# Kernel optimization log

Hardware: AMD Instinct MI355X
Metric: run time of the kernel (lower is better)

## Reference

```python
import jax, jax.numpy as jnp
import numpy as np

EMBED_DIM = 1024
NUM_HEADS = 16
HEAD_DIM = EMBED_DIM // NUM_HEADS


def setup_inputs() -> dict:
    key = jax.random.key(0)
    ks = jax.random.split(key, 9)
    s = 1.0 / np.sqrt(EMBED_DIM)
    inp = {"x": jax.random.normal(ks[0], (2, 2048, EMBED_DIM), dtype=jnp.float32)}
    for i, name in enumerate(["q", "k", "v", "out"]):
        inp[f"W_{name}"] = jax.random.uniform(ks[1 + 2 * i], (EMBED_DIM, EMBED_DIM), jnp.float32, -s, s)
        inp[f"b_{name}"] = jax.random.uniform(ks[2 + 2 * i], (EMBED_DIM,), jnp.float32, -s, s)
    return inp


def _heads(x):
    # [B, S, D] -> [B, H, S, Dh]
    b, s, _ = x.shape
    return x.reshape(b, s, NUM_HEADS, HEAD_DIM).transpose(0, 2, 1, 3)


def reference(x, W_q, b_q, W_k, b_k, W_v, b_v, W_out, b_out):
    q = _heads(x @ W_q.T + b_q)
    k = _heads(x @ W_k.T + b_k)
    v = _heads(x @ W_v.T + b_v)
    scale = HEAD_DIM ** 0.5
    logits = jnp.einsum("bhqd,bhkd->bhqk", q, k) / scale  # [B,H,S,S]
    s = x.shape[1]
    causal = jnp.tril(jnp.ones((s, s), dtype=bool))
    logits = jnp.where(causal, logits, -jnp.inf)
    a = jax.nn.softmax(logits, axis=-1)
    o = jnp.einsum("bhqk,bhkd->bhqd", a, v)
    o = o.transpose(0, 2, 1, 3).reshape(x.shape[0], s, EMBED_DIM)
    return o @ W_out.T + b_out
```

## Files before the change

### kernel.cpp

```cpp
#include <hip/hip_runtime.h>
#include <hip/hip_bf16.h>

typedef __bf16 bf16_t;
typedef __bf16 bf16x8 __attribute__((ext_vector_type(8)));
typedef __bf16 bf16x4 __attribute__((ext_vector_type(4)));
typedef float  f32x4  __attribute__((ext_vector_type(4)));

#define MFMA16(a, b, c) __builtin_amdgcn_mfma_f32_16x16x32_bf16((a), (b), (c), 0, 0, 0)

constexpr int E  = 1024;
constexpr int S  = 2048;
constexpr int H  = 16;
constexpr int M  = 4096;

__device__ __forceinline__ void glds16(const bf16_t* src, bf16_t* dst) {
  __builtin_amdgcn_global_load_lds(
      (const __attribute__((address_space(1))) void*)src,
      (__attribute__((address_space(3))) void*)dst, 16, 0, 0);
}

template <int ROWS, int NT>
__device__ __forceinline__ void stage_tile(const bf16_t* g, int gld,
                                           bf16_t* lds, int tid) {
  const int w = tid >> 6, l = tid & 63;
#pragma unroll
  for (int i = 0; i < ROWS * 8 / NT; ++i) {
    const int c = i * NT + w * 64 + l;
    const int row = c >> 3;
    const int gch = (c & 7) ^ (row & 7);
    glds16(g + (size_t)row * gld + gch * 8, lds + (size_t)(i * NT + w * 64) * 8);
  }
}

__device__ __forceinline__ bf16x8 read_frag(const bf16_t* lds, int row, int kc) {
  return *(const bf16x8*)(lds + (size_t)((row << 3) + (kc ^ (row & 7))) * 8);
}

__global__ void cvt_all_kernel(const float* __restrict__ x,
                               const float* __restrict__ w0, const float* __restrict__ w1,
                               const float* __restrict__ w2, const float* __restrict__ w3,
                               bf16_t* __restrict__ xb,
                               bf16_t* __restrict__ o0, bf16_t* __restrict__ o1,
                               bf16_t* __restrict__ o2, bf16_t* __restrict__ o3) {
  const int bid = blockIdx.x;
  const float* s;
  bf16_t* d;
  int idx;
  if (bid < 4096) {
    s = x; d = xb; idx = bid * 256 + threadIdx.x;
  } else {
    const int seg = (bid - 4096) >> 10;
    s = seg == 0 ? w0 : seg == 1 ? w1 : seg == 2 ? w2 : w3;
    d = seg == 0 ? o0 : seg == 1 ? o1 : seg == 2 ? o2 : o3;
    idx = ((bid - 4096) & 1023) * 256 + threadIdx.x;
  }
  float4 v = ((const float4*)s)[idx];
  bf16x4 o;
  o[0] = (bf16_t)v.x; o[1] = (bf16_t)v.y; o[2] = (bf16_t)v.z; o[3] = (bf16_t)v.w;
  ((bf16x4*)d)[idx] = o;
}

__device__ __forceinline__ void gemm_core(const bf16_t* __restrict__ A,
                                          const bf16_t* __restrict__ W, int Kd,
                                          bf16_t* As, bf16_t* Bs, int tid,
                                          f32x4 acc[4][4]) {
  const int w = tid >> 6, l = tid & 63;
  const int lq = l & 15, qd = l >> 4;
  const int wr = (w >> 1) * 64, wc = (w & 1) * 64;
#pragma unroll
  for (int i = 0; i < 4; ++i)
#pragma unroll
    for (int j = 0; j < 4; ++j) acc[i][j] = (f32x4){0.f, 0.f, 0.f, 0.f};

  const int KT = Kd / 64;
  for (int kt = 0; kt < KT; ++kt) {
    __syncthreads();
    stage_tile<128, 256>(A + kt * 64, Kd, As, tid);
    stage_tile<128, 256>(W + kt * 64, Kd, Bs, tid);
    __syncthreads();
#pragma unroll
    for (int ks = 0; ks < 2; ++ks) {
      bf16x8 af[4], bw[4];
#pragma unroll
      for (int mi = 0; mi < 4; ++mi)
        af[mi] = read_frag(As, wr + mi * 16 + lq, ks * 4 + qd);
#pragma unroll
      for (int ni = 0; ni < 4; ++ni)
        bw[ni] = read_frag(Bs, wc + ni * 16 + lq, ks * 4 + qd);
#pragma unroll
      for (int mi = 0; mi < 4; ++mi)
#pragma unroll
        for (int ni = 0; ni < 4; ++ni)
          acc[mi][ni] = MFMA16(af[mi], bw[ni], acc[mi][ni]);
    }
  }
}

__global__ __launch_bounds__(256) void qkv_gemm_kernel(
    const bf16_t* __restrict__ xb,
    const bf16_t* __restrict__ wq, const bf16_t* __restrict__ wk,
    const bf16_t* __restrict__ wv,
    const float* __restrict__ bq, const float* __restrict__ bk,
    const float* __restrict__ bv,
    bf16_t* __restrict__ Qb, bf16_t* __restrict__ Kb, bf16_t* __restrict__ Vb) {
  __shared__ __align__(16) bf16_t As[128 * 64];
  __shared__ __align__(16) bf16_t Bs[128 * 64];
  const int tid = threadIdx.x;
  const int which = blockIdx.x >> 3;
  const int n0 = (blockIdx.x & 7) * 128;
  const int m0 = blockIdx.y * 128;
  const bf16_t* Wp = which == 0 ? wq : which == 1 ? wk : wv;
  const float* bp  = which == 0 ? bq : which == 1 ? bk : bv;
  bf16_t* Out      = which == 0 ? Qb : which == 1 ? Kb : Vb;
  const float sc = (which == 0) ? (1.4426950408889634f * 0.125f) : 1.0f;

  f32x4 acc[4][4];
  gemm_core(xb + (size_t)m0 * E, Wp + (size_t)n0 * E, E, As, Bs, tid, acc);

  const int w = tid >> 6, l = tid & 63, lq = l & 15, qd = l >> 4;
  const int wr = (w >> 1) * 64, wc = (w & 1) * 64;
#pragma unroll
  for (int ni = 0; ni < 4; ++ni) {
    const int col = n0 + wc + ni * 16 + lq;
    const float bvv = bp[col];
#pragma unroll
    for (int mi = 0; mi < 4; ++mi)
#pragma unroll
      for (int r = 0; r < 4; ++r) {
        const int row = m0 + wr + mi * 16 + qd * 4 + r;
        Out[(size_t)row * E + col] = (bf16_t)((acc[mi][ni][r] + bvv) * sc);
      }
  }
}

__global__ __launch_bounds__(256) void vtrans_kernel(const bf16_t* __restrict__ Vb,
                                                     bf16_t* __restrict__ VT) {
  constexpr int LDT = 72;
  __shared__ __align__(16) bf16_t T[64 * LDT];
  const int tid = threadIdx.x;
  const int st = blockIdx.x, bh = blockIdx.y;
  const int b = bh >> 4, h = bh & 15;
  const int s0 = st * 64;
  const size_t rowbase = (size_t)b * S;
#pragma unroll
  for (int i = 0; i < 2; ++i) {
    const int c = i * 256 + tid;
    const int sl = c >> 3, dp = c & 7;
    const int a = sl >> 4, bb = (sl >> 2) & 3, cc = sl & 3;
    const int p = (a >> 1) * 32 + bb * 8 + (a & 1) * 4 + cc;
    bf16x8 v = *(const bf16x8*)(Vb + (rowbase + s0 + sl) * E + h * 64 + dp * 8);
    *(bf16x8*)&T[p * LDT + dp * 8] = v;
  }
  __syncthreads();
#pragma unroll
  for (int i = 0; i < 2; ++i) {
    const int c = i * 256 + tid;
    const int d = c >> 3, pp = (c & 7) * 8;
    bf16x8 o;
#pragma unroll
    for (int j = 0; j < 8; ++j) o[j] = T[(pp + j) * LDT + d];
    *(bf16x8*)&VT[((size_t)bh * 64 + d) * S + s0 + pp] = o;
  }
}

__global__ __launch_bounds__(256) void oproj_gemm_kernel(
    const bf16_t* __restrict__ Ob, const bf16_t* __restrict__ wo,
    const float* __restrict__ bo, float* __restrict__ out) {
  __shared__ __align__(16) bf16_t As[64 * 64];
  __shared__ __align__(16) bf16_t Bs[128 * 64];
  const int tid = threadIdx.x;
  const int n0 = blockIdx.x * 128;
  const int m0 = blockIdx.y * 64;
  const int w = tid >> 6, l = tid & 63, lq = l & 15, qd = l >> 4;
  const int wr = (w >> 1) * 32, wc = (w & 1) * 64;

  f32x4 acc[2][4];
#pragma unroll
  for (int i = 0; i < 2; ++i)
#pragma unroll
    for (int j = 0; j < 4; ++j) acc[i][j] = (f32x4){0.f, 0.f, 0.f, 0.f};

  for (int kt = 0; kt < 16; ++kt) {
    __syncthreads();
    stage_tile<64, 256>(Ob + (size_t)m0 * E + kt * 64, E, As, tid);
    stage_tile<128, 256>(wo + (size_t)n0 * E + kt * 64, E, Bs, tid);
    __syncthreads();
#pragma unroll
    for (int ks = 0; ks < 2; ++ks) {
      bf16x8 af[2], bw[4];
#pragma unroll
      for (int mi = 0; mi < 2; ++mi)
        af[mi] = read_frag(As, wr + mi * 16 + lq, ks * 4 + qd);
#pragma unroll
      for (int ni = 0; ni < 4; ++ni)
        bw[ni] = read_frag(Bs, wc + ni * 16 + lq, ks * 4 + qd);
#pragma unroll
      for (int mi = 0; mi < 2; ++mi)
#pragma unroll
        for (int ni = 0; ni < 4; ++ni)
          acc[mi][ni] = MFMA16(af[mi], bw[ni], acc[mi][ni]);
    }
  }
#pragma unroll
  for (int ni = 0; ni < 4; ++ni) {
    const int col = n0 + wc + ni * 16 + lq;
    const float bvv = bo[col];
#pragma unroll
    for (int mi = 0; mi < 2; ++mi)
#pragma unroll
      for (int r = 0; r < 4; ++r) {
        const int row = m0 + wr + mi * 16 + qd * 4 + r;
        out[(size_t)row * E + col] = acc[mi][ni][r] + bvv;
      }
  }
}

__global__ __launch_bounds__(128, 2) void attn_kernel(
    const bf16_t* __restrict__ Q, const bf16_t* __restrict__ K,
    const bf16_t* __restrict__ VT, bf16_t* __restrict__ O) {
  __shared__ __align__(16) bf16_t Ks[2][64 * 64];
  __shared__ __align__(16) bf16_t Vt[2][64 * 64];

  const int tid = threadIdx.x;
  const int w = tid >> 6, l = tid & 63;
  const int lq = l & 15, qd = l >> 4;
  const int bid = blockIdx.x;
  const int g = bid & 7, t = bid >> 3;
  const int bh = g * 4 + (t & 3);
  const int qt = 31 - (t >> 2);
  const int b = bh >> 4, h = bh & 15;
  const int qr = qt * 64 + w * 32;
  const size_t rowbase = (size_t)b * S;
  const size_t vtbase = (size_t)bh * 64 * S;
  const bf16_t* Kg = K + rowbase * E + h * 64;
  const bf16_t* Vg = VT + vtbase;

  stage_tile<64, 128>(Kg, E, Ks[0], tid);
  stage_tile<64, 128>(Vg, S, Vt[0], tid);

  bf16x8 aq[2][2];
#pragma unroll
  for (int mi = 0; mi < 2; ++mi)
#pragma unroll
    for (int ks = 0; ks < 2; ++ks)
      aq[mi][ks] = *(const bf16x8*)(Q + (rowbase + qr + mi * 16 + lq) * E +
                                    h * 64 + ks * 32 + qd * 8);

  f32x4 oacc[2][4];
#pragma unroll
  for (int mi = 0; mi < 2; ++mi)
#pragma unroll
    for (int nt = 0; nt < 4; ++nt) oacc[mi][nt] = (f32x4){0.f, 0.f, 0.f, 0.f};
  float rs[2] = {0.f, 0.f};

  for (int kt = 0; kt <= qt; ++kt) {
    __syncthreads();
    if (kt < qt) {
      const int kn = (kt + 1) * 64;
      stage_tile<64, 128>(Kg + (size_t)kn * E, E, Ks[(kt + 1) & 1], tid);
      stage_tile<64, 128>(Vg + kn, S, Vt[(kt + 1) & 1], tid);
    }
    const bf16_t* Kc = Ks[kt & 1];
    const bf16_t* Vc = Vt[kt & 1];
    const int k0 = kt * 64;
    const bool needmask = (k0 + 63 > qr);

    f32x4 sacc[2][4];
#pragma unroll
    for (int mi = 0; mi < 2; ++mi)
#pragma unroll
      for (int nt = 0; nt < 4; ++nt) sacc[mi][nt] = (f32x4){0.f, 0.f, 0.f, 0.f};
#pragma unroll
    for (int ks = 0; ks < 2; ++ks) {
      bf16x8 bk[4];
#pragma unroll
      for (int nt = 0; nt < 4; ++nt)
        bk[nt] = read_frag(Kc, nt * 16 + lq, ks * 4 + qd);
#pragma unroll
      for (int mi = 0; mi < 2; ++mi)
#pragma unroll
        for (int nt = 0; nt < 4; ++nt)
          sacc[mi][nt] = MFMA16(bk[nt], aq[mi][ks], sacc[mi][nt]);
    }
    bf16x8 ap[2][2];
#pragma unroll
    for (int mi = 0; mi < 2; ++mi) {
#pragma unroll
      for (int nt = 0; nt < 4; ++nt)
#pragma unroll
        for (int r = 0; r < 4; ++r) {
          float pv = exp2f(sacc[mi][nt][r]);
          if (needmask) {
            const int kg = k0 + nt * 16 + qd * 4 + r;
            const int qg = qr + mi * 16 + lq;
            pv = (kg > qg) ? 0.f : pv;
          }
          rs[mi] += pv;
          ap[mi][nt >> 1][((nt & 1) << 2) | r] = (bf16_t)pv;
        }
    }
#pragma unroll
    for (int ks = 0; ks < 2; ++ks) {
      bf16x8 bv[4];
#pragma unroll
      for (int nt = 0; nt < 4; ++nt)
        bv[nt] = read_frag(Vc, nt * 16 + lq, ks * 4 + qd);
#pragma unroll
      for (int mi = 0; mi < 2; ++mi)
#pragma unroll
        for (int nt = 0; nt < 4; ++nt)
          oacc[mi][nt] = MFMA16(ap[mi][ks], bv[nt], oacc[mi][nt]);
    }
  }

#pragma unroll
  for (int mi = 0; mi < 2; ++mi) {
    float tt = rs[mi];
    tt += __shfl_xor(tt, 16);
    tt += __shfl_xor(tt, 32);
    rs[mi] = tt;
  }
#pragma unroll
  for (int mi = 0; mi < 2; ++mi) {
    float rinv[4];
#pragma unroll
    for (int r = 0; r < 4; ++r)
      rinv[r] = 1.0f / __shfl(rs[mi], qd * 4 + r);
#pragma unroll
    for (int nt = 0; nt < 4; ++nt)
#pragma unroll
      for (int r = 0; r < 4; ++r) {
        const int qg = qr + mi * 16 + qd * 4 + r;
        O[(rowbase + qg) * E + h * 64 + nt * 16 + lq] =
            (bf16_t)(oacc[mi][nt][r] * rinv[r]);
      }
  }
}

extern "C" void kernel_launch(void* const* d_in, const int* in_sizes, int n_in,
                              void* d_out, int out_size, void* d_ws, size_t ws_size,
                              hipStream_t stream) {
  const float* x  = (const float*)d_in[0];
  const float* Wq = (const float*)d_in[1];
  const float* bq = (const float*)d_in[2];
  const float* Wk = (const float*)d_in[3];
  const float* bk = (const float*)d_in[4];
  const float* Wv = (const float*)d_in[5];
  const float* bv = (const float*)d_in[6];
  const float* Wo = (const float*)d_in[7];
  const float* bo = (const float*)d_in[8];
  float* out = (float*)d_out;

  unsigned char* ws = (unsigned char*)d_ws;
  constexpr size_t MB = 1ull << 20;
  bf16_t* xb  = (bf16_t*)(ws + 0 * MB);
  bf16_t* wqb = (bf16_t*)(ws + 8 * MB);
  bf16_t* wkb = (bf16_t*)(ws + 10 * MB);
  bf16_t* wvb = (bf16_t*)(ws + 12 * MB);
  bf16_t* wob = (bf16_t*)(ws + 14 * MB);
  bf16_t* Qb  = (bf16_t*)(ws + 16 * MB);
  bf16_t* Kb  = (bf16_t*)(ws + 24 * MB);
  bf16_t* Vb  = (bf16_t*)(ws + 32 * MB);
  bf16_t* VT  = (bf16_t*)(ws + 40 * MB);
  bf16_t* Ob  = xb;

  cvt_all_kernel<<<4096 + 4 * 1024, 256, 0, stream>>>(
      x, Wq, Wk, Wv, Wo, xb, wqb, wkb, wvb, wob);

  qkv_gemm_kernel<<<dim3(24, 32), 256, 0, stream>>>(
      xb, wqb, wkb, wvb, bq, bk, bv, Qb, Kb, Vb);

  vtrans_kernel<<<dim3(32, 32), 256, 0, stream>>>(Vb, VT);

  attn_kernel<<<1024, 128, 0, stream>>>(Qb, Kb, VT, Ob);

  oproj_gemm_kernel<<<dim3(8, 64), 256, 0, stream>>>(Ob, wob, bo, out);
}
```

Baseline: 208.8 us.

## Pair causal query tiles per block and use four waves of 16 rows

```diff
diff --git a/kernel.cpp b/kernel.cpp
--- a/kernel.cpp
+++ b/kernel.cpp
@@ -215,7 +215,7 @@
   }
 }
 
-__global__ __launch_bounds__(128, 2) void attn_kernel(
+__global__ __launch_bounds__(256, 2) void attn_kernel(
     const bf16_t* __restrict__ Q, const bf16_t* __restrict__ K,
     const bf16_t* __restrict__ VT, bf16_t* __restrict__ O) {
   __shared__ __align__(16) bf16_t Ks[2][64 * 64];
@@ -227,112 +227,100 @@
   const int bid = blockIdx.x;
   const int g = bid & 7, t = bid >> 3;
   const int bh = g * 4 + (t & 3);
-  const int qt = 31 - (t >> 2);
+  const int p = t >> 2;
   const int b = bh >> 4, h = bh & 15;
-  const int qr = qt * 64 + w * 32;
   const size_t rowbase = (size_t)b * S;
-  const size_t vtbase = (size_t)bh * 64 * S;
   const bf16_t* Kg = K + rowbase * E + h * 64;
-  const bf16_t* Vg = VT + vtbase;
-
-  stage_tile<64, 128>(Kg, E, Ks[0], tid);
-  stage_tile<64, 128>(Vg, S, Vt[0], tid);
-
-  bf16x8 aq[2][2];
-#pragma unroll
-  for (int mi = 0; mi < 2; ++mi)
+  const bf16_t* Vg = VT + (size_t)bh * 64 * S;
+
+  stage_tile<64, 256>(Kg, E, Ks[0], tid);
+  stage_tile<64, 256>(Vg, S, Vt[0], tid);
+  int cb = 0;
+
+#pragma unroll 1
+  for (int seg = 0; seg < 2; ++seg) {
+    const int qt = seg ? p : 31 - p;
+    const int qr = qt * 64 + w * 16;
+
+    bf16x8 aq[2];
 #pragma unroll
     for (int ks = 0; ks < 2; ++ks)
-      aq[mi][ks] = *(const bf16x8*)(Q + (rowbase + qr + mi * 16 + lq) * E +
-                                    h * 64 + ks * 32 + qd * 8);
-
-  f32x4 oacc[2][4];
-#pragma unroll
-  for (int mi = 0; mi < 2; ++mi)
-#pragma unroll
-    for (int nt = 0; nt < 4; ++nt) oacc[mi][nt] = (f32x4){0.f, 0.f, 0.f, 0.f};
-  float rs[2] = {0.f, 0.f};
-
-  for (int kt = 0; kt <= qt; ++kt) {
-    __syncthreads();
-    if (kt < qt) {
-      const int kn = (kt + 1) * 64;
-      stage_tile<64, 128>(Kg + (size_t)kn * E, E, Ks[(kt + 1) & 1], tid);
-      stage_tile<64, 128>(Vg + kn, S, Vt[(kt + 1) & 1], tid);
-    }
-    const bf16_t* Kc = Ks[kt & 1];
-    const bf16_t* Vc = Vt[kt & 1];
-    const int k0 = kt * 64;
-    const bool needmask = (k0 + 63 > qr);
-
-    f32x4 sacc[2][4];
-#pragma unroll
-    for (int mi = 0; mi < 2; ++mi)
-#pragma unroll
-      for (int nt = 0; nt < 4; ++nt) sacc[mi][nt] = (f32x4){0.f, 0.f, 0.f, 0.f};
-#pragma unroll
-    for (int ks = 0; ks < 2; ++ks) {
-      bf16x8 bk[4];
+      aq[ks] = *(const bf16x8*)(Q + (rowbase + qr + lq) * E + h * 64 +
+                                ks * 32 + qd * 8);
+
+    f32x4 oacc[4];
+#pragma unroll
+    for (int nt = 0; nt < 4; ++nt) oacc[nt] = (f32x4){0.f, 0.f, 0.f, 0.f};
+    float rs4[4] = {0.f, 0.f, 0.f, 0.f};
+
+    for (int kt = 0; kt <= qt; ++kt) {
+      __syncthreads();
+      if (kt < qt) {
+        const int kn = (kt + 1) * 64;
+        stage_tile<64, 256>(Kg + (size_t)kn * E, E, Ks[cb ^ 1], tid);
+        stage_tile<64, 256>(Vg + kn, S, Vt[cb ^ 1], tid);
+      } else if (seg == 0) {
+        stage_tile<64, 256>(Kg, E, Ks[cb ^ 1], tid);
+        stage_tile<64, 256>(Vg, S, Vt[cb ^ 1], tid);
+      }
+      const bf16_t* Kc = Ks[cb];
+      const bf16_t* Vc = Vt[cb];
+      const int k0 = kt * 64;
+      const bool needmask = (kt == qt);
+
+      f32x4 sacc[4];
+#pragma unroll
+      for (int nt = 0; nt < 4; ++nt) sacc[nt] = (f32x4){0.f, 0.f, 0.f, 0.f};
+#pragma unroll
+      for (int ks = 0; ks < 2; ++ks) {
+        bf16x8 bk[4];
+#pragma unroll
+        for (int nt = 0; nt < 4; ++nt)
+          bk[nt] = read_frag(Kc, nt * 16 + lq, ks * 4 + qd);
+#pragma unroll
+        for (int nt = 0; nt < 4; ++nt)
+          sacc[nt] = MFMA16(bk[nt], aq[ks], sacc[nt]);
+      }
+      bf16x8 ap[2];
 #pragma unroll
       for (int nt = 0; nt < 4; ++nt)
-        bk[nt] = read_frag(Kc, nt * 16 + lq, ks * 4 + qd);
-#pragma unroll
-      for (int mi = 0; mi < 2; ++mi)
-#pragma unroll
-        for (int nt = 0; nt < 4; ++nt)
-          sacc[mi][nt] = MFMA16(bk[nt], aq[mi][ks], sacc[mi][nt]);
-    }
-    bf16x8 ap[2][2];
-#pragma unroll
-    for (int mi = 0; mi < 2; ++mi) {
-#pragma unroll
-      for (int nt = 0; nt < 4; ++nt)
 #pragma unroll
         for (int r = 0; r < 4; ++r) {
-          float pv = exp2f(sacc[mi][nt][r]);
+          float pv = exp2f(sacc[nt][r]);
           if (needmask) {
             const int kg = k0 + nt * 16 + qd * 4 + r;
-            const int qg = qr + mi * 16 + lq;
+            const int qg = qr + lq;
             pv = (kg > qg) ? 0.f : pv;
           }
-          rs[mi] += pv;
-          ap[mi][nt >> 1][((nt & 1) << 2) | r] = (bf16_t)pv;
+          rs4[nt] += pv;
+          ap[nt >> 1][((nt & 1) << 2) | r] = (bf16_t)pv;
         }
+#pragma unroll
+      for (int ks = 0; ks < 2; ++ks) {
+        bf16x8 bv[4];
+#pragma unroll
+        for (int nt = 0; nt < 4; ++nt)
+          bv[nt] = read_frag(Vc, nt * 16 + lq, ks * 4 + qd);
+#pragma unroll
+        for (int nt = 0; nt < 4; ++nt)
+          oacc[nt] = MFMA16(ap[ks], bv[nt], oacc[nt]);
+      }
+      cb ^= 1;
     }
-#pragma unroll
-    for (int ks = 0; ks < 2; ++ks) {
-      bf16x8 bv[4];
-#pragma unroll
-      for (int nt = 0; nt < 4; ++nt)
-        bv[nt] = read_frag(Vc, nt * 16 + lq, ks * 4 + qd);
-#pragma unroll
-      for (int mi = 0; mi < 2; ++mi)
-#pragma unroll
-        for (int nt = 0; nt < 4; ++nt)
-          oacc[mi][nt] = MFMA16(ap[mi][ks], bv[nt], oacc[mi][nt]);
-    }
-  }
-
-#pragma unroll
-  for (int mi = 0; mi < 2; ++mi) {
-    float tt = rs[mi];
-    tt += __shfl_xor(tt, 16);
-    tt += __shfl_xor(tt, 32);
-    rs[mi] = tt;
-  }
-#pragma unroll
-  for (int mi = 0; mi < 2; ++mi) {
+
+    float rs = (rs4[0] + rs4[1]) + (rs4[2] + rs4[3]);
+    rs += __shfl_xor(rs, 16);
+    rs += __shfl_xor(rs, 32);
     float rinv[4];
 #pragma unroll
-    for (int r = 0; r < 4; ++r)
-      rinv[r] = 1.0f / __shfl(rs[mi], qd * 4 + r);
+    for (int r = 0; r < 4; ++r) rinv[r] = 1.0f / __shfl(rs, qd * 4 + r);
 #pragma unroll
     for (int nt = 0; nt < 4; ++nt)
 #pragma unroll
       for (int r = 0; r < 4; ++r) {
-        const int qg = qr + mi * 16 + qd * 4 + r;
+        const int qg = qr + qd * 4 + r;
         O[(rowbase + qg) * E + h * 64 + nt * 16 + lq] =
-            (bf16_t)(oacc[mi][nt][r] * rinv[r]);
+            (bf16_t)(oacc[nt][r] * rinv[r]);
       }
   }
 }
@@ -372,7 +360,7 @@
 
   vtrans_kernel<<<dim3(32, 32), 256, 0, stream>>>(Vb, VT);
 
-  attn_kernel<<<1024, 128, 0, stream>>>(Qb, Kb, VT, Ob);
+  attn_kernel<<<512, 256, 0, stream>>>(Qb, Kb, VT, Ob);
 
   oproj_gemm_kernel<<<dim3(8, 64), 256, 0, stream>>>(Ob, wob, bo, out);
 }
```

Result: faster. 190.6 us (-8.7%).
